# Performance work log

Hardware: AMD Instinct MI355X
Metric: run time of the kernel (lower is better)

Reference implementation:

```python
import jax, jax.numpy as jnp
import numpy as np
from jax import lax

E = 1024      # embed_dim
H = 16        # num_heads
HD = E // H   # head_dim = 64
GS = 2        # head_group_size
G = H // GS   # num head groups = 8
KQ = 3        # kq kernel q size
KK = 3        # kq kernel k size


def setup_inputs() -> dict:
    key = jax.random.key(0)
    ks = jax.random.split(key, 18)
    B, S = 2, 1024
    def rn(k, shape, scale=1.0):
        return jax.random.normal(k, shape, dtype=jnp.float32) * scale
    return {
        "Q": rn(ks[0], (B, S, E)),
        "K": rn(ks[1], (B, S, E)),
        "V": rn(ks[2], (B, S, E)),
        "Wq": rn(ks[3], (E, E), 0.02), "bq": rn(ks[4], (E,), 0.02),
        "Wk": rn(ks[5], (E, E), 0.02), "bk": rn(ks[6], (E,), 0.02),
        "Wv": rn(ks[7], (E, E), 0.02), "bv": rn(ks[8], (E,), 0.02),
        "Wo": rn(ks[9], (E, E), 0.02), "bo": rn(ks[10], (E,), 0.02),
        # depthwise key-query conv: [out=H, in/groups=1, KQ, KK]
        "kq_w": rn(ks[11], (H, 1, KQ, KK), 0.1),
        "kq_b": rn(ks[12], (H,), 0.02),
        # grouped 1x1 head-mix conv: weight [H, GS] (kernel dim squeezed), bias [H]
        "mix_w": rn(ks[13], (H, GS), 0.3),
        "mix_b": rn(ks[14], (H,), 0.02),
        # DynamicTanh params over head_dim (channels_last)
        "dyt_alpha": jnp.array([0.5], dtype=jnp.float32),
        "dyt_w": jnp.ones((HD,), dtype=jnp.float32),
        "dyt_b": jnp.zeros((HD,), dtype=jnp.float32),
        "depth_scale": jnp.ones((1,), dtype=jnp.float32),
    }


def reference(Q, K, V, Wq, bq, Wk, bk, Wv, bv, Wo, bo,
              kq_w, kq_b, mix_w, mix_b, dyt_alpha, dyt_w, dyt_b, depth_scale):
    B, S, _ = Q.shape
    scale = HD ** (-0.5)
    # projections -> [B, H, S, HD]
    q = (Q @ Wq + bq).reshape(B, S, H, HD).transpose(0, 2, 1, 3)
    k = (K @ Wk + bk).reshape(B, S, H, HD).transpose(0, 2, 1, 3)
    v = (V @ Wv + bv).reshape(B, S, H, HD).transpose(0, 2, 1, 3)

    # raw logits [B, H, Sq, Sk], multiplicative causal mask (zeros above diag)
    logits = jnp.einsum('bhqd,bhkd->bhqk', q, k) * scale
    causal = jnp.tril(jnp.ones((S, S), dtype=logits.dtype))
    logits = logits * causal

    # per-head (depthwise) key-query conv2d; torch pads q-dim by 2 both sides
    # then crops to first S rows (causal in q), k-dim padded symmetrically by 1
    conv = lax.conv_general_dilated(
        logits, kq_w, window_strides=(1, 1),
        padding=[(KQ - 1, KQ - 1), ((KK - 1) // 2, (KK - 1) // 2)],
        dimension_numbers=('NCHW', 'OIHW', 'NCHW'),
        feature_group_count=H)
    conv = conv + kq_b[None, :, None, None]
    conv = conv[:, :, :S, :]

    attn = jax.nn.softmax(conv, axis=-1)

    # grouped 1x1 head-mixing conv (within groups of GS heads) + bias
    attn_g = attn.reshape(B, G, GS, S, S)
    mw = mix_w.reshape(G, GS, GS)  # [group, out_in_group, in_in_group]
    mixed = jnp.einsum('goj,bgjqk->bgoqk', mw, attn_g).reshape(B, H, S, S)
    mixed = mixed + mix_b[None, :, None, None]

    out = jnp.einsum('bhqk,bhkd->bhqd', mixed, v)
    # DynamicTanh over head_dim (channels_last) + depth scale
    out = jnp.tanh(dyt_alpha * out) * dyt_w + dyt_b
    out = out * depth_scale
    out = out.transpose(0, 2, 1, 3).reshape(B, S, E)
    return out @ Wo + bo
```

## Files before the change

kernel.cpp:

```cpp
#include <hip/hip_runtime.h>
#include <cstdint>
#include <cstddef>

typedef __bf16 bf16;
typedef __bf16 bf16x8 __attribute__((ext_vector_type(8)));
typedef float f32x4 __attribute__((ext_vector_type(4)));

#define DEVI static __device__ __forceinline__

DEVI unsigned int cvt_pk_bf16(float lo, float hi) {
  unsigned int bl = __float_as_uint(lo);
  bl += 0x7fffu + ((bl >> 16) & 1u);
  unsigned int bh = __float_as_uint(hi);
  bh += 0x7fffu + ((bh >> 16) & 1u);
  return (bl >> 16) | (bh & 0xffff0000u);
}
DEVI float bf_lo(unsigned int u) { return __uint_as_float(u << 16); }
DEVI float bf_hi(unsigned int u) { return __uint_as_float(u & 0xffff0000u); }

DEVI void gload16(const bf16* g, bf16* l) {
  __builtin_amdgcn_global_load_lds(
      (const __attribute__((address_space(1))) unsigned int*)g,
      (__attribute__((address_space(3))) unsigned int*)l, 16, 0, 0);
}

__global__ __launch_bounds__(256) void prep_k(
    const float* __restrict__ Wq, const float* __restrict__ Wk,
    const float* __restrict__ Wv, const float* __restrict__ Wo,
    const float* __restrict__ Q, const float* __restrict__ K,
    const float* __restrict__ V, bf16* __restrict__ Wt,
    bf16* __restrict__ Ab)
{
  __shared__ bf16 Ts[64 * 72];
  const int bid = blockIdx.x, tid = threadIdx.x;
  if (bid < 1024) {
    const int z = bid >> 8;
    const float* W = (z == 0) ? Wq : (z == 1) ? Wk : (z == 2) ? Wv : Wo;
    bf16* out = Wt + ((size_t)z << 20);
    const int n0 = (bid & 15) * 64, k0 = ((bid >> 4) & 15) * 64;
    #pragma unroll
    for (int i = 0; i < 4; ++i) {
      int t = tid + i * 256;
      int kr = t >> 4, nc = t & 15;
      float4 v = *(const float4*)(W + (size_t)(k0 + kr) * 1024 + n0 + nc * 4);
      Ts[(nc * 4 + 0) * 72 + kr] = (bf16)v.x;
      Ts[(nc * 4 + 1) * 72 + kr] = (bf16)v.y;
      Ts[(nc * 4 + 2) * 72 + kr] = (bf16)v.z;
      Ts[(nc * 4 + 3) * 72 + kr] = (bf16)v.w;
    }
    __syncthreads();
    const int n = tid >> 2, kc = tid & 3;
    *(uint4*)(out + (size_t)(n0 + n) * 1024 + k0 + kc * 16) =
        *(const uint4*)(&Ts[n * 72 + kc * 16]);
    *(uint4*)(out + (size_t)(n0 + n) * 1024 + k0 + kc * 16 + 8) =
        *(const uint4*)(&Ts[n * 72 + kc * 16 + 8]);
  } else {
    const int t = bid - 1024;
    const int z = t >> 10, x = t & 1023;
    const float* A = (z == 0) ? Q : (z == 1) ? K : V;
    bf16* o = Ab + ((size_t)z << 21);
    const size_t idx = (size_t)x * 256 + tid;
    const float4 v0 = *(const float4*)(A + idx * 8);
    const float4 v1 = *(const float4*)(A + idx * 8 + 4);
    uint4 u;
    u.x = cvt_pk_bf16(v0.x, v0.y);
    u.y = cvt_pk_bf16(v0.z, v0.w);
    u.z = cvt_pk_bf16(v1.x, v1.y);
    u.w = cvt_pk_bf16(v1.z, v1.w);
    *(uint4*)(o + idx * 8) = u;
  }
}

__global__ __launch_bounds__(256) void proj_gemm_k(
    const bf16* __restrict__ Ab, const bf16* __restrict__ Wt,
    const float* __restrict__ bq, const float* __restrict__ bk,
    const float* __restrict__ bv, bf16* __restrict__ outbase,
    float* __restrict__ Tsum)
{
  const int z = blockIdx.z;
  const bf16* A  = Ab + ((size_t)z << 21);
  const bf16* Bt = Wt + ((size_t)z << 20);
  const float* bias = (z == 0) ? bq : (z == 1) ? bk : bv;
  bf16* outb = outbase + ((size_t)z << 21);

  __shared__ __align__(16) bf16 Asm[2][8192];
  __shared__ __align__(16) bf16 Bsm[2][4096];

  const int tid = threadIdx.x, lane = tid & 63, wid = tid >> 6;
  const int q4 = lane >> 4, n16 = lane & 15;
  const int wm = wid >> 1, wn = wid & 1;
  const int bid = blockIdx.x;
  const int m0 = (bid & 15) * 128, n0 = (bid >> 4) * 64;

  const int cbase = wid * 64 + lane;
  const bf16* gA[4];
  #pragma unroll
  for (int i = 0; i < 4; ++i) {
    int cc = cbase + i * 256;
    gA[i] = A + (size_t)(m0 + (cc >> 3)) * 1024 + (((cc & 7) ^ ((cc >> 3) & 7)) << 3);
  }
  const bf16* gB[2];
  #pragma unroll
  for (int i = 0; i < 2; ++i) {
    int cc = cbase + i * 256;
    gB[i] = Bt + (size_t)(n0 + (cc >> 3)) * 1024 + (((cc & 7) ^ ((cc >> 3) & 7)) << 3);
  }
  const int swl = n16 & 7;

  f32x4 acc[4][2] = {};

  #pragma unroll
  for (int i = 0; i < 4; ++i) gload16(gA[i], &Asm[0][i * 2048 + wid * 512]);
  #pragma unroll
  for (int i = 0; i < 2; ++i) gload16(gB[i], &Bsm[0][i * 2048 + wid * 512]);
  __syncthreads();

  int cur = 0;
  for (int t = 0; t < 16; ++t) {
    if (t < 15) {
      const int kc = (t + 1) * 64;
      #pragma unroll
      for (int i = 0; i < 4; ++i) gload16(gA[i] + kc, &Asm[cur ^ 1][i * 2048 + wid * 512]);
      #pragma unroll
      for (int i = 0; i < 2; ++i) gload16(gB[i] + kc, &Bsm[cur ^ 1][i * 2048 + wid * 512]);
    }
    const char* ab = (const char*)&Asm[cur][0];
    const char* bb = (const char*)&Bsm[cur][0];
    bf16x8 af[2][4], bfv[2][2];
    #pragma unroll
    for (int kk2 = 0; kk2 < 2; ++kk2) {
      #pragma unroll
      for (int rt = 0; rt < 4; ++rt)
        af[kk2][rt] = *(const bf16x8*)(ab + (wm * 64 + rt * 16 + n16) * 128 +
                                       (((kk2 * 4 + q4) ^ swl) << 4));
      #pragma unroll
      for (int ct = 0; ct < 2; ++ct)
        bfv[kk2][ct] = *(const bf16x8*)(bb + (wn * 32 + ct * 16 + n16) * 128 +
                                        (((kk2 * 4 + q4) ^ swl) << 4));
    }
    #pragma unroll
    for (int kk2 = 0; kk2 < 2; ++kk2)
      #pragma unroll
      for (int rt = 0; rt < 4; ++rt)
        #pragma unroll
        for (int ct = 0; ct < 2; ++ct)
          acc[rt][ct] = __builtin_amdgcn_mfma_f32_16x16x32_bf16(af[kk2][rt], bfv[kk2][ct], acc[rt][ct], 0, 0, 0);
    __syncthreads();
    cur ^= 1;
  }

  if (z < 2) {
    const int h = n0 >> 6;
    #pragma unroll
    for (int ct = 0; ct < 2; ++ct) {
      const int dl = wn * 32 + ct * 16 + n16;
      const float bvl = bias[n0 + dl];
      #pragma unroll
      for (int rt = 0; rt < 4; ++rt) {
        #pragma unroll
        for (int r = 0; r < 4; ++r) {
          int row = m0 + wm * 64 + rt * 16 + q4 * 4 + r;
          int b2 = row >> 10, s = row & 1023;
          outb[((size_t)((b2 * 16 + h) * 1024 + s) << 6) + dl] =
              (bf16)(acc[rt][ct][r] + bvl);
        }
      }
    }
  } else {
    const int b2 = m0 >> 10, kt0 = (m0 & 1023) >> 6, hh = n0 >> 6;
    bf16* vout = outb + ((size_t)(b2 * 16 + hh) << 16) + (size_t)(kt0 + wm) * 4096;
    float csum[2] = {0.f, 0.f};
    #pragma unroll
    for (int rt = 0; rt < 4; ++rt) {
      const int kk = rt >> 1;
      const int q4c = (rt & 1) * 2 + (q4 >> 1);
      const int jo = (q4 & 1) * 4;
      #pragma unroll
      for (int ct = 0; ct < 2; ++ct) {
        const int cl = wn * 32 + ct * 16 + n16;
        const float bvl = bias[n0 + cl];
        unsigned int p0 = cvt_pk_bf16(acc[rt][ct][0] + bvl, acc[rt][ct][1] + bvl);
        unsigned int p1 = cvt_pk_bf16(acc[rt][ct][2] + bvl, acc[rt][ct][3] + bvl);
        csum[ct] += bf_lo(p0) + bf_hi(p0) + bf_lo(p1) + bf_hi(p1);
        *(uint2*)(vout + kk * 2048 + (wn * 2 + ct) * 512 + (q4c * 16 + n16) * 8 + jo) =
            make_uint2(p0, p1);
      }
    }
    #pragma unroll
    for (int ct = 0; ct < 2; ++ct) {
      csum[ct] += __shfl_xor(csum[ct], 16);
      csum[ct] += __shfl_xor(csum[ct], 32);
    }
    if (lane < 16) {
      float* tsd = Tsum + ((size_t)(b2 * 16 + hh) * 16 + kt0 + wm) * 64 + wn * 32 + n16;
      tsd[0]  = csum[0];
      tsd[16] = csum[1];
    }
  }
}

__global__ __launch_bounds__(256) void out_gemm_k(
    const bf16* __restrict__ Ab, const bf16* __restrict__ Bt,
    const float* __restrict__ bias, float* __restrict__ outf)
{
  __shared__ __align__(16) bf16 Asm[2][4096];
  __shared__ __align__(16) bf16 Bsm[2][4096];
  const int tid = threadIdx.x, lane = tid & 63, wid = tid >> 6;
  const int q4 = lane >> 4, n16 = lane & 15;
  const int wm = wid >> 1, wn = wid & 1;
  const int bid = blockIdx.x;
  const int m0 = (bid & 31) * 64, n0 = (bid >> 5) * 64;
  const int cbase = wid * 64 + lane;
  const bf16* gA[2];
  const bf16* gB[2];
  #pragma unroll
  for (int i = 0; i < 2; ++i) {
    int cc = cbase + i * 256;
    gA[i] = Ab + (size_t)(m0 + (cc >> 3)) * 1024 + (((cc & 7) ^ ((cc >> 3) & 7)) << 3);
    gB[i] = Bt + (size_t)(n0 + (cc >> 3)) * 1024 + (((cc & 7) ^ ((cc >> 3) & 7)) << 3);
  }
  const int swl = n16 & 7;
  f32x4 acc[2][2] = {};

  #pragma unroll
  for (int i = 0; i < 2; ++i) {
    gload16(gA[i], &Asm[0][i * 2048 + wid * 512]);
    gload16(gB[i], &Bsm[0][i * 2048 + wid * 512]);
  }
  __syncthreads();

  int cur = 0;
  for (int t = 0; t < 16; ++t) {
    if (t < 15) {
      const int kc = (t + 1) * 64;
      #pragma unroll
      for (int i = 0; i < 2; ++i) {
        gload16(gA[i] + kc, &Asm[cur ^ 1][i * 2048 + wid * 512]);
        gload16(gB[i] + kc, &Bsm[cur ^ 1][i * 2048 + wid * 512]);
      }
    }
    const char* ab = (const char*)&Asm[cur][0];
    const char* bb = (const char*)&Bsm[cur][0];
    bf16x8 af[2][2], bfv[2][2];
    #pragma unroll
    for (int kk2 = 0; kk2 < 2; ++kk2) {
      #pragma unroll
      for (int rt = 0; rt < 2; ++rt)
        af[kk2][rt] = *(const bf16x8*)(ab + (wm * 32 + rt * 16 + n16) * 128 +
                                       (((kk2 * 4 + q4) ^ swl) << 4));
      #pragma unroll
      for (int ct = 0; ct < 2; ++ct)
        bfv[kk2][ct] = *(const bf16x8*)(bb + (wn * 32 + ct * 16 + n16) * 128 +
                                        (((kk2 * 4 + q4) ^ swl) << 4));
    }
    #pragma unroll
    for (int kk2 = 0; kk2 < 2; ++kk2)
      #pragma unroll
      for (int rt = 0; rt < 2; ++rt)
        #pragma unroll
        for (int ct = 0; ct < 2; ++ct)
          acc[rt][ct] = __builtin_amdgcn_mfma_f32_16x16x32_bf16(af[kk2][rt], bfv[kk2][ct], acc[rt][ct], 0, 0, 0);
    __syncthreads();
    cur ^= 1;
  }
  #pragma unroll
  for (int ct = 0; ct < 2; ++ct) {
    int col = n0 + wn * 32 + ct * 16 + n16;
    float bvl = bias[col];
    #pragma unroll
    for (int rt = 0; rt < 2; ++rt)
      #pragma unroll
      for (int r = 0; r < 4; ++r) {
        int row = m0 + wm * 32 + rt * 16 + q4 * 4 + r;
        outf[(size_t)row * 1024 + col] = acc[rt][ct][r] + bvl;
      }
  }
}

__global__ __launch_bounds__(320) void logits_conv_k(
    const bf16* __restrict__ qh, const bf16* __restrict__ kh,
    const float* __restrict__ kq_w, const float* __restrict__ kq_b,
    bf16* __restrict__ conv_out, float* __restrict__ tstats,
    const float* __restrict__ Tsum, float* __restrict__ Vtail)
{
  const int tt = blockIdx.x;
  const int h = blockIdx.y, b = blockIdx.z;
  if (tt == 151) {
    const int d = threadIdx.x;
    if (d < 64) {
      float* vt = Vtail + (size_t)(b * 16 + h) * 17 * 64;
      vt[16 * 64 + d] = 0.f;
      float c = 0.f;
      for (int kt = 15; kt >= 0; --kt) {
        c += Tsum[((size_t)(b * 16 + h) * 16 + kt) * 64 + d];
        vt[kt * 64 + d] = c;
      }
    }
    return;
  }
  int qt = 0, base = 0;
  while (qt < 15 && base + qt + 2 <= tt) { base += qt + 2; ++qt; }
  const int ct = tt - base;
  const int q0 = qt * 64, c0 = ct * 64;
  __shared__ __align__(16) char un[19456];
  bf16* Kst = (bf16*)un;
  float* Ls = (float*)un;
  const int tid = threadIdx.x;
  const int lane = tid & 63, wid = tid >> 6;
  const int q4 = lane >> 4, n16 = lane & 15;
  const bf16* qb = qh + ((size_t)(b * 16 + h) << 16);
  const bf16* kb = kh + ((size_t)(b * 16 + h) << 16);

  const int ar = min(max(q0 - 2 + wid * 16 + n16, 0), 1023);
  bf16x8 a0 = *(const bf16x8*)(qb + ar * 64 + q4 * 8);
  bf16x8 a1 = *(const bf16x8*)(qb + ar * 64 + 32 + q4 * 8);

  for (int t = tid; t < 640; t += 320) {
    int row = t >> 3, ch = t & 7;
    int br = min(max(c0 - 1 + row, 0), 1023);
    *(uint4*)(&Kst[row * 72 + ch * 8]) = *(const uint4*)(kb + br * 64 + ch * 8);
  }
  __syncthreads();

  f32x4 acc[5] = {};
  #pragma unroll
  for (int c5 = 0; c5 < 5; ++c5) {
    int brow = c5 * 16 + n16;
    bf16x8 b0 = *(const bf16x8*)(&Kst[brow * 72 + q4 * 8]);
    bf16x8 b1 = *(const bf16x8*)(&Kst[brow * 72 + 32 + q4 * 8]);
    acc[c5] = __builtin_amdgcn_mfma_f32_16x16x32_bf16(a0, b0, acc[c5], 0, 0, 0);
    acc[c5] = __builtin_amdgcn_mfma_f32_16x16x32_bf16(a1, b1, acc[c5], 0, 0, 0);
  }
  __syncthreads();

  #pragma unroll
  for (int c5 = 0; c5 < 5; ++c5) {
    #pragma unroll
    for (int r = 0; r < 4; ++r) {
      int Lrow = wid * 16 + q4 * 4 + r;
      int Lcol = c5 * 16 + n16;
      if (Lrow < 66 && Lcol < 66) {
        int rg = q0 - 2 + Lrow;
        int cg = c0 - 1 + Lcol;
        float v = (cg >= 0 && cg <= rg) ? acc[c5][r] * 0.125f : 0.f;
        Ls[Lrow * 72 + Lcol] = v;
      }
    }
  }
  __syncthreads();

  if (tid < 256) {
    float w9[9];
    #pragma unroll
    for (int i = 0; i < 9; ++i) w9[i] = kq_w[h * 9 + i];
    const float bb = kq_b[h];
    const size_t tplane = (size_t)(b * 16 + h) * 151 + base + ct;
    bf16* tb = conv_out + tplane * 4096;
    float2* st = (float2*)tstats + tplane * 64;

    const int r = tid >> 2, qr = tid & 3;
    float4 R0[5], R1[5], R2[5];
    const float* L0 = &Ls[r * 72 + qr * 16];
    #pragma unroll
    for (int i = 0; i < 5; ++i) {
      R0[i] = *(const float4*)(L0 + i * 4);
      R1[i] = *(const float4*)(L0 + 72 + i * 4);
      R2[i] = *(const float4*)(L0 + 144 + i * 4);
    }
    const float* f0 = (const float*)R0;
    const float* f1 = (const float*)R1;
    const float* f2 = (const float*)R2;
    float o[16];
    #pragma unroll
    for (int jj = 0; jj < 16; ++jj)
      o[jj] = bb + w9[0]*f0[jj] + w9[1]*f0[jj+1] + w9[2]*f0[jj+2]
                 + w9[3]*f1[jj] + w9[4]*f1[jj+1] + w9[5]*f1[jj+2]
                 + w9[6]*f2[jj] + w9[7]*f2[jj+1] + w9[8]*f2[jj+2];
    float mx = o[0];
    #pragma unroll
    for (int jj = 1; jj < 16; ++jj) mx = fmaxf(mx, o[jj]);
    mx = fmaxf(mx, __shfl_xor(mx, 1));
    mx = fmaxf(mx, __shfl_xor(mx, 2));
    unsigned int p[8];
    #pragma unroll
    for (int jj = 0; jj < 8; ++jj)
      p[jj] = cvt_pk_bf16(__expf(o[2*jj] - mx), __expf(o[2*jj+1] - mx));
    const int kk = qr >> 1, q4b = (qr & 1) * 2, sr = r >> 4, n16r = r & 15;
    *(uint4*)(tb + (sr * 2 + kk) * 512 + (q4b * 16 + n16r) * 8)       = *(const uint4*)&p[0];
    *(uint4*)(tb + (sr * 2 + kk) * 512 + ((q4b + 1) * 16 + n16r) * 8) = *(const uint4*)&p[4];
    float s = 0.f;
    #pragma unroll
    for (int jj = 0; jj < 8; ++jj) s += bf_lo(p[jj]) + bf_hi(p[jj]);
    s += __shfl_xor(s, 1);
    s += __shfl_xor(s, 2);
    if (qr == 0) st[r] = make_float2(mx, s);
  }
}

__global__ __launch_bounds__(256) void pv_k(
    const bf16* __restrict__ conv_out, const bf16* __restrict__ V2,
    const float* __restrict__ tstats, const float* __restrict__ Vtail,
    const float* __restrict__ mix_w, const float* __restrict__ mix_b,
    const float* __restrict__ kq_b,
    const float* __restrict__ dyt_alpha, const float* __restrict__ dyt_w,
    const float* __restrict__ dyt_b, const float* __restrict__ depth_scale,
    bf16* __restrict__ out_attn)
{
  const int qt16 = blockIdx.x, g = blockIdx.y, b = blockIdx.z;
  const int qt = qt16 >> 2;
  const int nkt = min(qt + 2, 16);
  const int Tc = 1024 - (nkt << 6);
  const int tid = threadIdx.x, lane = tid & 63, wid = tid >> 6;
  const int q4 = lane >> 4, n16 = lane & 15;
  const int oo = wid >> 1, kh = wid & 1;
  const int h0 = 2 * g, ho = h0 + oo;
  const int sr = qt16 & 3, strow = sr * 16;
  const size_t tbase = (size_t)(qt * (qt + 3) / 2);

  __shared__ float2 rsS[2][16];
  if (tid < 32) {
    const int hh = tid >> 4, rw = tid & 15;
    const float2* tsp = (const float2*)tstats +
        ((size_t)(b * 16 + h0 + hh) * 151 + tbase) * 64 + strow + rw;
    const float kb2 = kq_b[h0 + hh];
    float mx = (Tc > 0) ? kb2 : -3.0e38f;
    for (int kt = 0; kt < nkt; ++kt) mx = fmaxf(mx, tsp[(size_t)kt * 64].x);
    float s = (float)Tc * __expf(kb2 - mx);
    for (int kt = 0; kt < nkt; ++kt) {
      float2 v = tsp[(size_t)kt * 64];
      s += v.y * __expf(v.x - mx);
    }
    rsS[hh][rw] = make_float2(mx, 1.f / s);
  }
  __syncthreads();

  const float2 r0 = rsS[0][n16];
  const float2 r1 = rsS[1][n16];
  const float m0 = r0.x, m1 = r1.x;
  const float mwa = mix_w[ho * 2 + 0], mwb = mix_w[ho * 2 + 1];
  const float wa = mwa * r0.y, wb = mwb * r1.y;

  const bf16* pb0 = conv_out +
      ((size_t)(b * 16 + h0) * 151 + tbase) * 4096 + sr * 1024 + lane * 8;
  const bf16* pb1 = pb0 + (size_t)151 * 4096;
  const float2* ts0 = (const float2*)tstats +
      ((size_t)(b * 16 + h0) * 151 + tbase) * 64 + strow + n16;
  const float2* ts1 = ts0 + (size_t)151 * 64;
  const bf16* vb = V2 + ((size_t)(b * 16 + ho) << 16) + lane * 8;

  const int niter = (nkt - kh + 1) >> 1;
  float wk0[8], wk1[8];
  #pragma unroll
  for (int i = 0; i < 8; ++i) {
    int ktc = (i < niter) ? (kh + 2 * i) : 0;
    wk0[i] = wa * __expf(ts0[(size_t)ktc * 64].x - m0);
    wk1[i] = wb * __expf(ts1[(size_t)ktc * 64].x - m1);
  }

  f32x4 acc[4] = {};
  int ii = 0;
  for (int kt = kh; kt < nkt; kt += 2, ++ii) {
    uint4 u0[2], u1[2];
    #pragma unroll
    for (int kk = 0; kk < 2; ++kk) {
      u0[kk] = *(const uint4*)(pb0 + (size_t)kt * 4096 + kk * 512);
      u1[kk] = *(const uint4*)(pb1 + (size_t)kt * 4096 + kk * 512);
    }
    bf16x8 bv[2][4];
    #pragma unroll
    for (int kk = 0; kk < 2; ++kk)
      #pragma unroll
      for (int ctt = 0; ctt < 4; ++ctt)
        bv[kk][ctt] = *(const bf16x8*)(vb + (size_t)kt * 4096 + kk * 2048 + ctt * 512);
    const float w0 = wk0[ii], w1 = wk1[ii];
    #pragma unroll
    for (int kk = 0; kk < 2; ++kk) {
      bf16x8 af;
      const unsigned int* a0p = (const unsigned int*)&u0[kk];
      const unsigned int* a1p = (const unsigned int*)&u1[kk];
      #pragma unroll
      for (int i2 = 0; i2 < 4; ++i2) {
        float a0 = w0 * bf_lo(a0p[i2]) + w1 * bf_lo(a1p[i2]);
        float a1 = w0 * bf_hi(a0p[i2]) + w1 * bf_hi(a1p[i2]);
        ((unsigned int*)&af)[i2] = cvt_pk_bf16(a0, a1);
      }
      #pragma unroll
      for (int ctt = 0; ctt < 4; ++ctt)
        acc[ctt] = __builtin_amdgcn_mfma_f32_16x16x32_bf16(af, bv[kk][ctt], acc[ctt], 0, 0, 0);
    }
  }

  __shared__ float Pp[2][16][64];
  if (kh == 1) {
    #pragma unroll
    for (int ctt = 0; ctt < 4; ++ctt)
      #pragma unroll
      for (int r = 0; r < 4; ++r)
        Pp[oo][q4 * 4 + r][ctt * 16 + n16] = acc[ctt][r];
  }
  __syncthreads();
  if (kh == 1) return;
  #pragma unroll
  for (int ctt = 0; ctt < 4; ++ctt)
    #pragma unroll
    for (int r = 0; r < 4; ++r)
      acc[ctt][r] += Pp[oo][q4 * 4 + r][ctt * 16 + n16];

  const float kqb0 = kq_b[h0], kqb1 = kq_b[h0 + 1];
  float tw[4];
  #pragma unroll
  for (int r = 0; r < 4; ++r) {
    float2 s0 = rsS[0][q4 * 4 + r];
    float2 s1 = rsS[1][q4 * 4 + r];
    tw[r] = (Tc > 0) ? (mwa * s0.y * __expf(kqb0 - s0.x) +
                        mwb * s1.y * __expf(kqb1 - s1.x)) : 0.f;
  }
  const float mb = mix_b[ho];
  const float alpha = dyt_alpha[0], dsc = depth_scale[0];
  const float* vt = Vtail + (size_t)(b * 16 + ho) * 17 * 64;
  #pragma unroll
  for (int ctt = 0; ctt < 4; ++ctt) {
    int d = ctt * 16 + n16;
    float vtn = vt[(size_t)nkt * 64 + d];
    float vt0 = vt[d];
    float wgt = dyt_w[d], bds = dyt_b[d];
    #pragma unroll
    for (int r = 0; r < 4; ++r) {
      float v = acc[ctt][r] + tw[r] * vtn + mb * vt0;
      float e = __expf(2.f * alpha * v);
      float th = 1.f - 2.f / (e + 1.f);
      float y = (th * wgt + bds) * dsc;
      int qr = qt16 * 16 + q4 * 4 + r;
      out_attn[(((size_t)(b * 1024 + qr)) << 10) + ho * 64 + d] = (bf16)y;
    }
  }
}

extern "C" void kernel_launch(void* const* d_in, const int* in_sizes, int n_in,
                              void* d_out, int out_size, void* d_ws, size_t ws_size,
                              hipStream_t stream) {
  const float* Q    = (const float*)d_in[0];
  const float* Kx   = (const float*)d_in[1];
  const float* V    = (const float*)d_in[2];
  const float* Wq   = (const float*)d_in[3];
  const float* bq   = (const float*)d_in[4];
  const float* Wk   = (const float*)d_in[5];
  const float* bk   = (const float*)d_in[6];
  const float* Wv   = (const float*)d_in[7];
  const float* bv   = (const float*)d_in[8];
  const float* Wo   = (const float*)d_in[9];
  const float* bo   = (const float*)d_in[10];
  const float* kq_w = (const float*)d_in[11];
  const float* kq_b = (const float*)d_in[12];
  const float* mixw = (const float*)d_in[13];
  const float* mixb = (const float*)d_in[14];
  const float* dyta = (const float*)d_in[15];
  const float* dytw = (const float*)d_in[16];
  const float* dytb = (const float*)d_in[17];
  const float* dsc  = (const float*)d_in[18];

  char* ws = (char*)d_ws;
  bf16* qh     = (bf16*)(ws);
  float* tstat = (float*)(ws + (size_t)(12 << 20));
  float* Vtail = (float*)(ws + (size_t)(16 << 20));
  float* Tsum  = (float*)(ws + (size_t)(16 << 20) + (256 << 10));
  bf16* WtT    = (bf16*)(ws + (size_t)(17 << 20));
  bf16* oat    = (bf16*)(ws + (size_t)(17 << 20));
  bf16* conv   = (bf16*)(ws + (size_t)(25 << 20));
  bf16* Ab     = (bf16*)(ws + (size_t)(25 << 20));
  bf16* kh     = qh + ((size_t)1 << 21);
  bf16* V2     = qh + ((size_t)2 << 21);

  prep_k<<<dim3(4096), 256, 0, stream>>>(Wq, Wk, Wv, Wo, Q, Kx, V, WtT, Ab);
  proj_gemm_k<<<dim3(256, 1, 3), 256, 0, stream>>>(Ab, WtT, bq, bk, bv, qh, Tsum);
  logits_conv_k<<<dim3(152, 16, 2), 320, 0, stream>>>(qh, kh, kq_w, kq_b, conv, tstat,
                                                      Tsum, Vtail);
  pv_k<<<dim3(64, 8, 2), 256, 0, stream>>>(conv, V2, tstat, Vtail, mixw, mixb, kq_b,
                                           dyta, dytw, dytb, dsc, oat);
  out_gemm_k<<<dim3(512), 256, 0, stream>>>(oat, WtT + ((size_t)3 << 20), bo, (float*)d_out);
}
```

Baseline: 204.5 us.

## Split PV key tiles across four warps, compute both mixed heads per warp

Result: slower. 209.6 us (+2.5%).

```diff
diff --git a/kernel.cpp b/kernel.cpp
--- a/kernel.cpp
+++ b/kernel.cpp
@@ -412,8 +412,7 @@
   const int Tc = 1024 - (nkt << 6);
   const int tid = threadIdx.x, lane = tid & 63, wid = tid >> 6;
   const int q4 = lane >> 4, n16 = lane & 15;
-  const int oo = wid >> 1, kh = wid & 1;
-  const int h0 = 2 * g, ho = h0 + oo;
+  const int h0 = 2 * g;
   const int sr = qt16 & 3, strow = sr * 16;
   const size_t tbase = (size_t)(qt * (qt + 3) / 2);
 
@@ -434,11 +433,10 @@
   }
   __syncthreads();
 
-  const float2 r0 = rsS[0][n16];
-  const float2 r1 = rsS[1][n16];
-  const float m0 = r0.x, m1 = r1.x;
-  const float mwa = mix_w[ho * 2 + 0], mwb = mix_w[ho * 2 + 1];
-  const float wa = mwa * r0.y, wb = mwb * r1.y;
+  const float m0v = rsS[0][n16].x, m1v = rsS[1][n16].x;
+  const float ri0 = rsS[0][n16].y, ri1 = rsS[1][n16].y;
+  const float c00 = mix_w[(h0 + 0) * 2 + 0] * ri0, c01 = mix_w[(h0 + 0) * 2 + 1] * ri1;
+  const float c10 = mix_w[(h0 + 1) * 2 + 0] * ri0, c11 = mix_w[(h0 + 1) * 2 + 1] * ri1;
 
   const bf16* pb0 = conv_out +
       ((size_t)(b * 16 + h0) * 151 + tbase) * 4096 + sr * 1024 + lane * 8;
@@ -446,94 +444,83 @@
   const float2* ts0 = (const float2*)tstats +
       ((size_t)(b * 16 + h0) * 151 + tbase) * 64 + strow + n16;
   const float2* ts1 = ts0 + (size_t)151 * 64;
-  const bf16* vb = V2 + ((size_t)(b * 16 + ho) << 16) + lane * 8;
-
-  const int niter = (nkt - kh + 1) >> 1;
-  float wk0[8], wk1[8];
-  #pragma unroll
-  for (int i = 0; i < 8; ++i) {
-    int ktc = (i < niter) ? (kh + 2 * i) : 0;
-    wk0[i] = wa * __expf(ts0[(size_t)ktc * 64].x - m0);
-    wk1[i] = wb * __expf(ts1[(size_t)ktc * 64].x - m1);
-  }
-
-  f32x4 acc[4] = {};
-  int ii = 0;
-  for (int kt = kh; kt < nkt; kt += 2, ++ii) {
+  const bf16* vb0 = V2 + ((size_t)(b * 16 + h0) << 16) + lane * 8;
+  const bf16* vb1 = vb0 + ((size_t)1 << 16);
+
+  f32x4 acc0[4] = {}, acc1[4] = {};
+  for (int kt = wid; kt < nkt; kt += 4) {
     uint4 u0[2], u1[2];
     #pragma unroll
     for (int kk = 0; kk < 2; ++kk) {
       u0[kk] = *(const uint4*)(pb0 + (size_t)kt * 4096 + kk * 512);
       u1[kk] = *(const uint4*)(pb1 + (size_t)kt * 4096 + kk * 512);
     }
-    bf16x8 bv[2][4];
-    #pragma unroll
-    for (int kk = 0; kk < 2; ++kk)
-      #pragma unroll
-      for (int ctt = 0; ctt < 4; ++ctt)
-        bv[kk][ctt] = *(const bf16x8*)(vb + (size_t)kt * 4096 + kk * 2048 + ctt * 512);
-    const float w0 = wk0[ii], w1 = wk1[ii];
+    const float e0 = __expf(ts0[(size_t)kt * 64].x - m0v);
+    const float e1 = __expf(ts1[(size_t)kt * 64].x - m1v);
+    const float w00 = c00 * e0, w01 = c01 * e1;
+    const float w10 = c10 * e0, w11 = c11 * e1;
     #pragma unroll
     for (int kk = 0; kk < 2; ++kk) {
-      bf16x8 af;
+      bf16x8 bv0[4], bv1[4];
+      #pragma unroll
+      for (int ctt = 0; ctt < 4; ++ctt) {
+        bv0[ctt] = *(const bf16x8*)(vb0 + (size_t)kt * 4096 + kk * 2048 + ctt * 512);
+        bv1[ctt] = *(const bf16x8*)(vb1 + (size_t)kt * 4096 + kk * 2048 + ctt * 512);
+      }
+      bf16x8 af0, af1;
       const unsigned int* a0p = (const unsigned int*)&u0[kk];
       const unsigned int* a1p = (const unsigned int*)&u1[kk];
       #pragma unroll
       for (int i2 = 0; i2 < 4; ++i2) {
-        float a0 = w0 * bf_lo(a0p[i2]) + w1 * bf_lo(a1p[i2]);
-        float a1 = w0 * bf_hi(a0p[i2]) + w1 * bf_hi(a1p[i2]);
-        ((unsigned int*)&af)[i2] = cvt_pk_bf16(a0, a1);
-      }
-      #pragma unroll
-      for (int ctt = 0; ctt < 4; ++ctt)
-        acc[ctt] = __builtin_amdgcn_mfma_f32_16x16x32_bf16(af, bv[kk][ctt], acc[ctt], 0, 0, 0);
-    }
-  }
-
-  __shared__ float Pp[2][16][64];
-  if (kh == 1) {
-    #pragma unroll
-    for (int ctt = 0; ctt < 4; ++ctt)
-      #pragma unroll
-      for (int r = 0; r < 4; ++r)
-        Pp[oo][q4 * 4 + r][ctt * 16 + n16] = acc[ctt][r];
-  }
-  __syncthreads();
-  if (kh == 1) return;
+        const float plo = bf_lo(a0p[i2]), phi = bf_hi(a0p[i2]);
+        const float qlo = bf_lo(a1p[i2]), qhi = bf_hi(a1p[i2]);
+        ((unsigned int*)&af0)[i2] = cvt_pk_bf16(w00 * plo + w01 * qlo,
+                                                w00 * phi + w01 * qhi);
+        ((unsigned int*)&af1)[i2] = cvt_pk_bf16(w10 * plo + w11 * qlo,
+                                                w10 * phi + w11 * qhi);
+      }
+      #pragma unroll
+      for (int ctt = 0; ctt < 4; ++ctt) {
+        acc0[ctt] = __builtin_amdgcn_mfma_f32_16x16x32_bf16(af0, bv0[ctt], acc0[ctt], 0, 0, 0);
+        acc1[ctt] = __builtin_amdgcn_mfma_f32_16x16x32_bf16(af1, bv1[ctt], acc1[ctt], 0, 0, 0);
+      }
+    }
+  }
+
+  __shared__ float Ps[8][16][65];
   #pragma unroll
   for (int ctt = 0; ctt < 4; ++ctt)
     #pragma unroll
-    for (int r = 0; r < 4; ++r)
-      acc[ctt][r] += Pp[oo][q4 * 4 + r][ctt * 16 + n16];
-
+    for (int r = 0; r < 4; ++r) {
+      Ps[wid * 2 + 0][q4 * 4 + r][ctt * 16 + n16] = acc0[ctt][r];
+      Ps[wid * 2 + 1][q4 * 4 + r][ctt * 16 + n16] = acc1[ctt][r];
+    }
+  __syncthreads();
+
+  const int o = tid >> 7, rem = tid & 127, row = rem >> 3, cg = rem & 7;
+  const float2 sA = rsS[0][row], sB = rsS[1][row];
   const float kqb0 = kq_b[h0], kqb1 = kq_b[h0 + 1];
-  float tw[4];
-  #pragma unroll
-  for (int r = 0; r < 4; ++r) {
-    float2 s0 = rsS[0][q4 * 4 + r];
-    float2 s1 = rsS[1][q4 * 4 + r];
-    tw[r] = (Tc > 0) ? (mwa * s0.y * __expf(kqb0 - s0.x) +
-                        mwb * s1.y * __expf(kqb1 - s1.x)) : 0.f;
-  }
-  const float mb = mix_b[ho];
+  const float mwa = mix_w[(h0 + o) * 2 + 0], mwb = mix_w[(h0 + o) * 2 + 1];
+  const float twr = (Tc > 0) ? (mwa * sA.y * __expf(kqb0 - sA.x) +
+                                mwb * sB.y * __expf(kqb1 - sB.x)) : 0.f;
+  const float mb = mix_b[h0 + o];
   const float alpha = dyt_alpha[0], dsc = depth_scale[0];
-  const float* vt = Vtail + (size_t)(b * 16 + ho) * 17 * 64;
-  #pragma unroll
-  for (int ctt = 0; ctt < 4; ++ctt) {
-    int d = ctt * 16 + n16;
-    float vtn = vt[(size_t)nkt * 64 + d];
-    float vt0 = vt[d];
-    float wgt = dyt_w[d], bds = dyt_b[d];
-    #pragma unroll
-    for (int r = 0; r < 4; ++r) {
-      float v = acc[ctt][r] + tw[r] * vtn + mb * vt0;
-      float e = __expf(2.f * alpha * v);
-      float th = 1.f - 2.f / (e + 1.f);
-      float y = (th * wgt + bds) * dsc;
-      int qr = qt16 * 16 + q4 * 4 + r;
-      out_attn[(((size_t)(b * 1024 + qr)) << 10) + ho * 64 + d] = (bf16)y;
-    }
-  }
+  const float* vt = Vtail + (size_t)(b * 16 + h0 + o) * 17 * 64;
+  bf16 outv[8];
+  #pragma unroll
+  for (int j = 0; j < 8; ++j) {
+    const int d = cg * 8 + j;
+    float s = Ps[0 * 2 + o][row][d] + Ps[1 * 2 + o][row][d] +
+              Ps[2 * 2 + o][row][d] + Ps[3 * 2 + o][row][d];
+    float v = s + twr * vt[(size_t)nkt * 64 + d] + mb * vt[d];
+    float e = __expf(2.f * alpha * v);
+    float th = 1.f - 2.f / (e + 1.f);
+    float y = (th * dyt_w[d] + dyt_b[d]) * dsc;
+    outv[j] = (bf16)y;
+  }
+  const int qr = qt16 * 16 + row;
+  *(uint4*)(out_attn + (((size_t)(b * 1024 + qr)) << 10) + (h0 + o) * 64 + cg * 8) =
+      *(const uint4*)outv;
 }
 
 extern "C" void kernel_launch(void* const* d_in, const int* in_sizes, int n_in,
```
